# Kernel optimization log

Hardware: AMD Instinct MI355X
Metric: run time of the kernel (lower is better)

Reference implementation:

```python
import jax, jax.numpy as jnp
import numpy as np

N = 100000          # nodes (edges-as-nodes in ChiENN)
CIRCLE = 8          # circle_size
D_IN = 128
D_OUT = 128
K = 2               # k_neighbors -> padding = K - 1 = 1
PAD = K - 1


def setup_inputs() -> dict:
    key = jax.random.key(0)
    ks = jax.random.split(key, 8)
    x = jax.random.normal(ks[0], (N, D_IN), dtype=jnp.float32)
    # circle_index: per-row first `length` entries are valid node ids, tail is -1 padding
    lengths = jax.random.randint(ks[1], (N,), 0, CIRCLE + 1)  # 0..CIRCLE
    idx = jax.random.randint(ks[2], (N, CIRCLE), 0, N)
    pos = jnp.arange(CIRCLE)[None, :]
    circle_index = jnp.where(pos < lengths[:, None], idx, -1).astype(jnp.int64)
    s = 1.0 / np.sqrt(D_IN)
    w1 = jax.random.uniform(ks[3], (D_IN, D_OUT), jnp.float32, -s, s)
    b1 = jnp.zeros((D_OUT,), jnp.float32)
    w2 = jax.random.uniform(ks[4], (D_IN, D_OUT), jnp.float32, -s, s)
    b2 = jnp.zeros((D_OUT,), jnp.float32)
    sf = 1.0 / np.sqrt(D_OUT)
    wf = jax.random.uniform(ks[5], (D_OUT, D_OUT), jnp.float32, -sf, sf)
    bf = jnp.zeros((D_OUT,), jnp.float32)
    return {"x": x, "w1": w1, "b1": b1, "w2": w2, "b2": b2,
            "wf": wf, "bf": bf, "circle_index": circle_index}


def reference(x, w1, b1, w2, b2, wf, bf, circle_index):
    n, circle_size = circle_index.shape
    agg_id = 0.0  # aggregation_id_element for 'add'

    # per-shift embeddings of node features, each with a zero row prepended (index 0 = padding)
    embs = [x @ w1 + b1, x @ w2 + b2]                       # each [N, D]
    d = embs[0].shape[-1]
    zero_row = jnp.zeros((1, d), embs[0].dtype)
    embs = [jnp.concatenate([zero_row, e], axis=0) for e in embs]  # [N+1, D]

    mask_sum = jnp.sum(circle_index == -1, axis=-1)          # [N]
    in_degree = circle_size - mask_sum - PAD
    in_degree = jnp.where(mask_sum == circle_size, 0, in_degree)

    ci = circle_index.reshape(-1) + 1                        # [N*circle]  (-1 -> 0 = zero row)
    L = ci.shape[0]
    ci = jnp.concatenate([ci, jnp.zeros((PAD,), ci.dtype)])

    shifted = []
    for i, e in enumerate(embs):
        se = e[ci[i:i + L]]                                  # [L, D] circular-shifted gather
        # mask rows whose node in-degree <= shift i
        m = jnp.repeat(in_degree <= i, circle_size)[:, None]  # [L, 1]
        shifted.append(jnp.where(m, agg_id, se))
    msg = jnp.sum(jnp.stack(shifted, axis=-2), axis=-2)      # 'add' aggregation, [L, D]
    msg = msg.reshape(n, circle_size, d)

    msg_mask = jnp.arange(1, circle_size + 1)[None, :] <= in_degree[:, None]
    msg = msg[:, :-PAD, :]                                   # drop circular padding slots
    msg_mask = msg_mask[:, :-PAD]
    msg = jnp.where(msg_mask[..., None], msg, 0.0)
    msg = msg @ wf + bf                                      # final_embedding (Linear)
    return msg, msg_mask
```

## Files before the change

### kernel.cpp

```cpp
#include <hip/hip_runtime.h>
#include <stdint.h>

typedef short bf16x8 __attribute__((ext_vector_type(8)));
typedef float f32x4  __attribute__((ext_vector_type(4)));

__device__ __forceinline__ unsigned short f2bf(float f) {
    unsigned int u = __float_as_uint(f);
    u += 0x7FFFu + ((u >> 16) & 1u);
    return (unsigned short)(u >> 16);
}
__device__ __forceinline__ float bf2f(unsigned short h) {
    return __uint_as_float(((unsigned int)h) << 16);
}

__global__ void fuse_weights(const float* __restrict__ w1, const float* __restrict__ b1,
                             const float* __restrict__ w2, const float* __restrict__ b2,
                             const float* __restrict__ wf,
                             unsigned short* __restrict__ wcT,
                             float* __restrict__ cb)
{
    int mat = blockIdx.x / 129;
    int kk  = blockIdx.x % 129;
    int c   = threadIdx.x;
    const float* w = (mat == 0) ? w1 : w2;
    const float* b = (mat == 0) ? b1 : b2;
    float acc = 0.f;
    if (kk < 128) {
        #pragma unroll 8
        for (int j = 0; j < 128; ++j) acc += w[kk * 128 + j] * wf[j * 128 + c];
        wcT[mat * 16384 + c * 128 + kk] = f2bf(acc);
    } else {
        #pragma unroll 8
        for (int j = 0; j < 128; ++j) acc += b[j] * wf[j * 128 + c];
        cb[mat * 128 + c] = acc;
    }
}

#define WAVE_ROWS 32
__global__ __launch_bounds__(512) void gemm_g(
    const float* __restrict__ x, const unsigned short* __restrict__ wcT,
    const float* __restrict__ cb, unsigned short* __restrict__ g, int nrows)
{
    __shared__ uint4 ldsw[4096];

    int tid  = threadIdx.x;
    int lane = tid & 63;
    int wid  = tid >> 6;
    int r0   = (blockIdx.x * 8 + wid) * WAVE_ROWS;
    int lrow = lane & 15;
    int kg   = lane >> 4;
    int swz  = (lrow & 7) << 4;

    const uint4* w4 = (const uint4*)wcT;
    #pragma unroll
    for (int i = 0; i < 8; ++i) {
        int idx = tid + i * 512;
        uint4 v = w4[idx];
        int b   = idx << 4;
        int sb  = b ^ (((b >> 8) & 7) << 4);
        ldsw[sb >> 4] = v;
    }

    bf16x8 xf[2][4];
    #pragma unroll
    for (int t = 0; t < 2; ++t) {
        int row = r0 + t * 16 + lrow;
        bool v  = row < nrows;
        #pragma unroll
        for (int ks = 0; ks < 4; ++ks) {
            int k0 = ks * 32 + kg * 8;
            float4 p0 = v ? *(const float4*)(x + (size_t)row * 128 + k0)     : float4{0,0,0,0};
            float4 p1 = v ? *(const float4*)(x + (size_t)row * 128 + k0 + 4) : float4{0,0,0,0};
            bf16x8 f;
            f[0] = (short)f2bf(p0.x); f[1] = (short)f2bf(p0.y);
            f[2] = (short)f2bf(p0.z); f[3] = (short)f2bf(p0.w);
            f[4] = (short)f2bf(p1.x); f[5] = (short)f2bf(p1.y);
            f[6] = (short)f2bf(p1.z); f[7] = (short)f2bf(p1.w);
            xf[t][ks] = f;
        }
    }

    __syncthreads();
    if (r0 >= nrows) return;

    const char* lbase = (const char*)ldsw;
    #pragma unroll
    for (int mat = 0; mat < 2; ++mat) {
        unsigned short* gm = g + (size_t)mat * nrows * 128;
        int mb = mat * 32768;
        #pragma unroll 2
        for (int c = 0; c < 8; ++c) {
            int colb = mb + (c * 16 + lrow) * 256 + kg * 16;
            bf16x8 wfr[4];
            #pragma unroll
            for (int ks = 0; ks < 4; ++ks)
                wfr[ks] = *(const bf16x8*)(lbase + ((colb + ks * 64) ^ swz));
            f32x4 acc[2];
            #pragma unroll
            for (int t = 0; t < 2; ++t) acc[t] = f32x4{0,0,0,0};
            #pragma unroll
            for (int ks = 0; ks < 4; ++ks) {
                #pragma unroll
                for (int t = 0; t < 2; ++t)
                    acc[t] = __builtin_amdgcn_mfma_f32_16x16x32_bf16(wfr[ks], xf[t][ks], acc[t], 0,0,0);
            }
            float4 bias = *(const float4*)(cb + mat * 128 + c * 16 + kg * 4);
            #pragma unroll
            for (int t = 0; t < 2; ++t) {
                int xrow = r0 + t * 16 + lrow;
                if (xrow < nrows) {
                    ushort4 o;
                    o.x = f2bf(acc[t][0] + bias.x); o.y = f2bf(acc[t][1] + bias.y);
                    o.z = f2bf(acc[t][2] + bias.z); o.w = f2bf(acc[t][3] + bias.w);
                    *(ushort4*)(gm + (size_t)xrow * 128 + c * 16 + kg * 4) = o;
                }
            }
        }
    }
}

__global__ __launch_bounds__(256) void gather_out(
    const int* __restrict__ ci, const unsigned short* __restrict__ g,
    const float* __restrict__ bfv, float* __restrict__ out,
    float* __restrict__ maskout, int nnodes)
{
    int n    = (int)((blockIdx.x * blockDim.x + threadIdx.x) >> 6);
    int lane = threadIdx.x & 63;
    if (n >= nnodes) return;

    int civ = ci[n * 8 + (lane & 7)];
    unsigned long long bal = __ballot(civ == -1);
    int cnt = __popcll(bal & 0xFFull);
    int deg = (cnt == 8) ? 0 : (7 - cnt);

    int half = lane >> 5;
    int hl   = lane & 31;
    int d4   = hl * 4;
    float4 bfd = *(const float4*)(bfv + d4);
    const unsigned short* g1 = g;
    const unsigned short* g2 = g + (size_t)nnodes * 128;
    bool two = (deg >= 2);

    uint2 va[4], vb[4];
    #pragma unroll
    for (int c = 0; c < 4; ++c) {
        va[c] = uint2{0u, 0u};
        vb[c] = uint2{0u, 0u};
        if (2 * c < deg) {
            int r  = 2 * c + half;
            int i0 = __shfl(civ, r);
            int i1 = __shfl(civ, r + 1);
            bool m = (r < deg);
            va[c] = m          ? *(const uint2*)(g1 + (size_t)i0 * 128 + d4) : uint2{0u, 0u};
            vb[c] = (m && two) ? *(const uint2*)(g2 + (size_t)i1 * 128 + d4) : uint2{0u, 0u};
        }
    }

    size_t base = (size_t)n * 896;
    #pragma unroll
    for (int c = 0; c < 4; ++c) {
        f32x4 o;
        o[0] = bfd.x + bf2f((unsigned short)(va[c].x & 0xFFFFu)) + bf2f((unsigned short)(vb[c].x & 0xFFFFu));
        o[1] = bfd.y + bf2f((unsigned short)(va[c].x >> 16))     + bf2f((unsigned short)(vb[c].x >> 16));
        o[2] = bfd.z + bf2f((unsigned short)(va[c].y & 0xFFFFu)) + bf2f((unsigned short)(vb[c].y & 0xFFFFu));
        o[3] = bfd.w + bf2f((unsigned short)(va[c].y >> 16))     + bf2f((unsigned short)(vb[c].y >> 16));
        if (c < 3)
            __builtin_nontemporal_store(o, (f32x4*)(out + base + c * 256 + lane * 4));
        else if (half == 0)
            __builtin_nontemporal_store(o, (f32x4*)(out + base + 768 + hl * 4));
    }
    if (lane < 7)
        __builtin_nontemporal_store((lane < deg) ? 1.0f : 0.0f, maskout + n * 7 + lane);
}

extern "C" void kernel_launch(void* const* d_in, const int* in_sizes, int n_in,
                              void* d_out, int out_size, void* d_ws, size_t ws_size,
                              hipStream_t stream) {
    const float* x   = (const float*)d_in[0];
    const float* w1  = (const float*)d_in[1];
    const float* b1  = (const float*)d_in[2];
    const float* w2  = (const float*)d_in[3];
    const float* b2  = (const float*)d_in[4];
    const float* wf  = (const float*)d_in[5];
    const float* bfv = (const float*)d_in[6];
    const int*   ci  = (const int*)d_in[7];

    int nrows = in_sizes[0] / 128;

    size_t gbytes = (size_t)2 * nrows * 128 * 2;
    unsigned short* g   = (unsigned short*)d_ws;
    unsigned short* wcT = (unsigned short*)((char*)d_ws + ((gbytes + 255) & ~(size_t)255));
    float*          cb  = (float*)((char*)wcT + 2 * 128 * 128 * 2);

    fuse_weights<<<2 * 129, 128, 0, stream>>>(w1, b1, w2, b2, wf, wcT, cb);

    int nblk = (nrows + 8 * WAVE_ROWS - 1) / (8 * WAVE_ROWS);
    gemm_g<<<nblk, 512, 0, stream>>>(x, wcT, cb, g, nrows);

    int rows = nrows * 7;
    int cblk = (nrows * 64 + 255) / 256;
    float* out = (float*)d_out;
    gather_out<<<cblk, 256, 0, stream>>>(ci, g, bfv, out, out + (size_t)rows * 128, nrows);
}
```

Measured before the change: 112.1 us.

## Fuse three kernels into one persistent kernel with grid-wide barriers

Merges the weight-fusion, GEMM and gather kernels into a single persistent kernel launched with at most 448 blocks. The phases are separated by software grid barriers built on an atomic counter, which is reset by a memset before launch. The aim is to remove two kernel-launch gaps and the drain/fill between stages. In exchange it adds atomic spin-wait barriers, depends on every block being co-resident, and runs grid-stride loops with fewer blocks, which may lower gather parallelism.

```diff
diff --git a/kernel.cpp b/kernel.cpp
--- a/kernel.cpp
+++ b/kernel.cpp
@@ -13,164 +13,192 @@
     return __uint_as_float(((unsigned int)h) << 16);
 }
 
-__global__ void fuse_weights(const float* __restrict__ w1, const float* __restrict__ b1,
-                             const float* __restrict__ w2, const float* __restrict__ b2,
-                             const float* __restrict__ wf,
-                             unsigned short* __restrict__ wcT,
-                             float* __restrict__ cb)
-{
-    int mat = blockIdx.x / 129;
-    int kk  = blockIdx.x % 129;
-    int c   = threadIdx.x;
-    const float* w = (mat == 0) ? w1 : w2;
-    const float* b = (mat == 0) ? b1 : b2;
-    float acc = 0.f;
-    if (kk < 128) {
-        #pragma unroll 8
-        for (int j = 0; j < 128; ++j) acc += w[kk * 128 + j] * wf[j * 128 + c];
-        wcT[mat * 16384 + c * 128 + kk] = f2bf(acc);
-    } else {
-        #pragma unroll 8
-        for (int j = 0; j < 128; ++j) acc += b[j] * wf[j * 128 + c];
-        cb[mat * 128 + c] = acc;
-    }
-}
-
 #define WAVE_ROWS 32
-__global__ __launch_bounds__(512) void gemm_g(
-    const float* __restrict__ x, const unsigned short* __restrict__ wcT,
-    const float* __restrict__ cb, unsigned short* __restrict__ g, int nrows)
+
+__global__ __launch_bounds__(512, 4) void fused_all(
+    const float* __restrict__ x,
+    const float* __restrict__ w1, const float* __restrict__ b1,
+    const float* __restrict__ w2, const float* __restrict__ b2,
+    const float* __restrict__ wf, const float* __restrict__ bfv,
+    const int* __restrict__ ci,
+    unsigned short* __restrict__ wcT, float* __restrict__ cb,
+    unsigned short* __restrict__ gbuf,
+    float* __restrict__ out, float* __restrict__ maskout,
+    int nrows, int ntiles, int nblk, unsigned* __restrict__ bar)
 {
     __shared__ uint4 ldsw[4096];
-
     int tid  = threadIdx.x;
+    int bid  = blockIdx.x;
     int lane = tid & 63;
     int wid  = tid >> 6;
-    int r0   = (blockIdx.x * 8 + wid) * WAVE_ROWS;
-    int lrow = lane & 15;
-    int kg   = lane >> 4;
-    int swz  = (lrow & 7) << 4;
-
-    const uint4* w4 = (const uint4*)wcT;
-    #pragma unroll
-    for (int i = 0; i < 8; ++i) {
-        int idx = tid + i * 512;
-        uint4 v = w4[idx];
-        int b   = idx << 4;
-        int sb  = b ^ (((b >> 8) & 7) << 4);
-        ldsw[sb >> 4] = v;
-    }
-
-    bf16x8 xf[2][4];
-    #pragma unroll
-    for (int t = 0; t < 2; ++t) {
-        int row = r0 + t * 16 + lrow;
-        bool v  = row < nrows;
+
+    {
+        int tg = bid * 512 + tid;
+        if (tg < 258 * 128) {
+            int c   = tg & 127;
+            int job = tg >> 7;
+            int mat = (job >= 129) ? 1 : 0;
+            int kk  = job - mat * 129;
+            const float* w = mat ? w2 : w1;
+            const float* b = mat ? b2 : b1;
+            float acc = 0.f;
+            if (kk < 128) {
+                #pragma unroll 8
+                for (int j = 0; j < 128; ++j) acc += w[kk * 128 + j] * wf[j * 128 + c];
+                wcT[mat * 16384 + c * 128 + kk] = f2bf(acc);
+            } else {
+                #pragma unroll 8
+                for (int j = 0; j < 128; ++j) acc += b[j] * wf[j * 128 + c];
+                cb[mat * 128 + c] = acc;
+            }
+        }
+    }
+
+    __syncthreads();
+    if (tid == 0) {
+        __threadfence();
+        atomicAdd(bar, 1u);
+        while (__hip_atomic_load(bar, __ATOMIC_RELAXED, __HIP_MEMORY_SCOPE_AGENT)
+               < (unsigned)nblk)
+            __builtin_amdgcn_s_sleep(1);
+        __threadfence();
+    }
+    __syncthreads();
+
+    {
+        int lrow = lane & 15;
+        int kg   = lane >> 4;
+        int swz  = (lrow & 7) << 4;
+
+        const uint4* w4 = (const uint4*)wcT;
         #pragma unroll
-        for (int ks = 0; ks < 4; ++ks) {
-            int k0 = ks * 32 + kg * 8;
-            float4 p0 = v ? *(const float4*)(x + (size_t)row * 128 + k0)     : float4{0,0,0,0};
-            float4 p1 = v ? *(const float4*)(x + (size_t)row * 128 + k0 + 4) : float4{0,0,0,0};
-            bf16x8 f;
-            f[0] = (short)f2bf(p0.x); f[1] = (short)f2bf(p0.y);
-            f[2] = (short)f2bf(p0.z); f[3] = (short)f2bf(p0.w);
-            f[4] = (short)f2bf(p1.x); f[5] = (short)f2bf(p1.y);
-            f[6] = (short)f2bf(p1.z); f[7] = (short)f2bf(p1.w);
-            xf[t][ks] = f;
-        }
-    }
-
-    __syncthreads();
-    if (r0 >= nrows) return;
-
-    const char* lbase = (const char*)ldsw;
-    #pragma unroll
-    for (int mat = 0; mat < 2; ++mat) {
-        unsigned short* gm = g + (size_t)mat * nrows * 128;
-        int mb = mat * 32768;
-        #pragma unroll 2
-        for (int c = 0; c < 8; ++c) {
-            int colb = mb + (c * 16 + lrow) * 256 + kg * 16;
-            bf16x8 wfr[4];
-            #pragma unroll
-            for (int ks = 0; ks < 4; ++ks)
-                wfr[ks] = *(const bf16x8*)(lbase + ((colb + ks * 64) ^ swz));
-            f32x4 acc[2];
-            #pragma unroll
-            for (int t = 0; t < 2; ++t) acc[t] = f32x4{0,0,0,0};
-            #pragma unroll
-            for (int ks = 0; ks < 4; ++ks) {
+        for (int i = 0; i < 8; ++i) {
+            int idx = tid + i * 512;
+            uint4 v = w4[idx];
+            int b   = idx << 4;
+            int sb  = b ^ (((b >> 8) & 7) << 4);
+            ldsw[sb >> 4] = v;
+        }
+        __syncthreads();
+        const char* lbase = (const char*)ldsw;
+
+        for (int tile = bid; tile < ntiles; tile += nblk) {
+            int r0 = tile * 256 + wid * WAVE_ROWS;
+            if (r0 >= nrows) continue;
+
+            bf16x8 xf[2][4];
+            #pragma unroll
+            for (int t = 0; t < 2; ++t) {
+                int row = r0 + t * 16 + lrow;
+                bool v  = row < nrows;
                 #pragma unroll
-                for (int t = 0; t < 2; ++t)
-                    acc[t] = __builtin_amdgcn_mfma_f32_16x16x32_bf16(wfr[ks], xf[t][ks], acc[t], 0,0,0);
-            }
-            float4 bias = *(const float4*)(cb + mat * 128 + c * 16 + kg * 4);
-            #pragma unroll
-            for (int t = 0; t < 2; ++t) {
-                int xrow = r0 + t * 16 + lrow;
-                if (xrow < nrows) {
-                    ushort4 o;
-                    o.x = f2bf(acc[t][0] + bias.x); o.y = f2bf(acc[t][1] + bias.y);
-                    o.z = f2bf(acc[t][2] + bias.z); o.w = f2bf(acc[t][3] + bias.w);
-                    *(ushort4*)(gm + (size_t)xrow * 128 + c * 16 + kg * 4) = o;
+                for (int ks = 0; ks < 4; ++ks) {
+                    int k0 = ks * 32 + kg * 8;
+                    float4 p0 = v ? *(const float4*)(x + (size_t)row * 128 + k0)     : float4{0,0,0,0};
+                    float4 p1 = v ? *(const float4*)(x + (size_t)row * 128 + k0 + 4) : float4{0,0,0,0};
+                    bf16x8 f;
+                    f[0] = (short)f2bf(p0.x); f[1] = (short)f2bf(p0.y);
+                    f[2] = (short)f2bf(p0.z); f[3] = (short)f2bf(p0.w);
+                    f[4] = (short)f2bf(p1.x); f[5] = (short)f2bf(p1.y);
+                    f[6] = (short)f2bf(p1.z); f[7] = (short)f2bf(p1.w);
+                    xf[t][ks] = f;
                 }
             }
-        }
-    }
-}
-
-__global__ __launch_bounds__(256) void gather_out(
-    const int* __restrict__ ci, const unsigned short* __restrict__ g,
-    const float* __restrict__ bfv, float* __restrict__ out,
-    float* __restrict__ maskout, int nnodes)
-{
-    int n    = (int)((blockIdx.x * blockDim.x + threadIdx.x) >> 6);
-    int lane = threadIdx.x & 63;
-    if (n >= nnodes) return;
-
-    int civ = ci[n * 8 + (lane & 7)];
-    unsigned long long bal = __ballot(civ == -1);
-    int cnt = __popcll(bal & 0xFFull);
-    int deg = (cnt == 8) ? 0 : (7 - cnt);
-
-    int half = lane >> 5;
-    int hl   = lane & 31;
-    int d4   = hl * 4;
-    float4 bfd = *(const float4*)(bfv + d4);
-    const unsigned short* g1 = g;
-    const unsigned short* g2 = g + (size_t)nnodes * 128;
-    bool two = (deg >= 2);
-
-    uint2 va[4], vb[4];
-    #pragma unroll
-    for (int c = 0; c < 4; ++c) {
-        va[c] = uint2{0u, 0u};
-        vb[c] = uint2{0u, 0u};
-        if (2 * c < deg) {
-            int r  = 2 * c + half;
-            int i0 = __shfl(civ, r);
-            int i1 = __shfl(civ, r + 1);
-            bool m = (r < deg);
-            va[c] = m          ? *(const uint2*)(g1 + (size_t)i0 * 128 + d4) : uint2{0u, 0u};
-            vb[c] = (m && two) ? *(const uint2*)(g2 + (size_t)i1 * 128 + d4) : uint2{0u, 0u};
-        }
-    }
-
-    size_t base = (size_t)n * 896;
-    #pragma unroll
-    for (int c = 0; c < 4; ++c) {
-        f32x4 o;
-        o[0] = bfd.x + bf2f((unsigned short)(va[c].x & 0xFFFFu)) + bf2f((unsigned short)(vb[c].x & 0xFFFFu));
-        o[1] = bfd.y + bf2f((unsigned short)(va[c].x >> 16))     + bf2f((unsigned short)(vb[c].x >> 16));
-        o[2] = bfd.z + bf2f((unsigned short)(va[c].y & 0xFFFFu)) + bf2f((unsigned short)(vb[c].y & 0xFFFFu));
-        o[3] = bfd.w + bf2f((unsigned short)(va[c].y >> 16))     + bf2f((unsigned short)(vb[c].y >> 16));
-        if (c < 3)
-            __builtin_nontemporal_store(o, (f32x4*)(out + base + c * 256 + lane * 4));
-        else if (half == 0)
-            __builtin_nontemporal_store(o, (f32x4*)(out + base + 768 + hl * 4));
-    }
-    if (lane < 7)
-        __builtin_nontemporal_store((lane < deg) ? 1.0f : 0.0f, maskout + n * 7 + lane);
+
+            #pragma unroll
+            for (int mat = 0; mat < 2; ++mat) {
+                unsigned short* gm = gbuf + (size_t)mat * nrows * 128;
+                int mb = mat * 32768;
+                #pragma unroll 2
+                for (int c = 0; c < 8; ++c) {
+                    int colb = mb + (c * 16 + lrow) * 256 + kg * 16;
+                    bf16x8 wfr[4];
+                    #pragma unroll
+                    for (int ks = 0; ks < 4; ++ks)
+                        wfr[ks] = *(const bf16x8*)(lbase + ((colb + ks * 64) ^ swz));
+                    f32x4 acc[2];
+                    #pragma unroll
+                    for (int t = 0; t < 2; ++t) acc[t] = f32x4{0,0,0,0};
+                    #pragma unroll
+                    for (int ks = 0; ks < 4; ++ks) {
+                        #pragma unroll
+                        for (int t = 0; t < 2; ++t)
+                            acc[t] = __builtin_amdgcn_mfma_f32_16x16x32_bf16(wfr[ks], xf[t][ks], acc[t], 0,0,0);
+                    }
+                    float4 bias = *(const float4*)(cb + mat * 128 + c * 16 + kg * 4);
+                    #pragma unroll
+                    for (int t = 0; t < 2; ++t) {
+                        int xrow = r0 + t * 16 + lrow;
+                        if (xrow < nrows) {
+                            ushort4 o;
+                            o.x = f2bf(acc[t][0] + bias.x); o.y = f2bf(acc[t][1] + bias.y);
+                            o.z = f2bf(acc[t][2] + bias.z); o.w = f2bf(acc[t][3] + bias.w);
+                            *(ushort4*)(gm + (size_t)xrow * 128 + c * 16 + kg * 4) = o;
+                        }
+                    }
+                }
+            }
+        }
+    }
+
+    __syncthreads();
+    if (tid == 0) {
+        __threadfence();
+        atomicAdd(bar, 1u);
+        while (__hip_atomic_load(bar, __ATOMIC_RELAXED, __HIP_MEMORY_SCOPE_AGENT)
+               < (unsigned)(2 * nblk))
+            __builtin_amdgcn_s_sleep(1);
+        __threadfence();
+    }
+    __syncthreads();
+
+    {
+        const unsigned short* g1 = gbuf;
+        const unsigned short* g2 = gbuf + (size_t)nrows * 128;
+        int half = lane >> 5;
+        int hl   = lane & 31;
+        int d4   = hl * 4;
+        float4 bfd = *(const float4*)(bfv + d4);
+
+        for (int n = bid * 8 + wid; n < nrows; n += nblk * 8) {
+            int civ = ci[n * 8 + (lane & 7)];
+            unsigned long long bal = __ballot(civ == -1);
+            int cnt = __popcll(bal & 0xFFull);
+            int deg = (cnt == 8) ? 0 : (7 - cnt);
+            bool two = (deg >= 2);
+
+            uint2 va[4], vb[4];
+            #pragma unroll
+            for (int c = 0; c < 4; ++c) {
+                va[c] = uint2{0u, 0u};
+                vb[c] = uint2{0u, 0u};
+                if (2 * c < deg) {
+                    int r  = 2 * c + half;
+                    int i0 = __shfl(civ, r);
+                    int i1 = __shfl(civ, r + 1);
+                    bool m = (r < deg);
+                    va[c] = m          ? *(const uint2*)(g1 + (size_t)i0 * 128 + d4) : uint2{0u, 0u};
+                    vb[c] = (m && two) ? *(const uint2*)(g2 + (size_t)i1 * 128 + d4) : uint2{0u, 0u};
+                }
+            }
+
+            size_t base = (size_t)n * 896;
+            #pragma unroll
+            for (int c = 0; c < 4; ++c) {
+                f32x4 o;
+                o[0] = bfd.x + bf2f((unsigned short)(va[c].x & 0xFFFFu)) + bf2f((unsigned short)(vb[c].x & 0xFFFFu));
+                o[1] = bfd.y + bf2f((unsigned short)(va[c].x >> 16))     + bf2f((unsigned short)(vb[c].x >> 16));
+                o[2] = bfd.z + bf2f((unsigned short)(va[c].y & 0xFFFFu)) + bf2f((unsigned short)(vb[c].y & 0xFFFFu));
+                o[3] = bfd.w + bf2f((unsigned short)(va[c].y >> 16))     + bf2f((unsigned short)(vb[c].y >> 16));
+                if (c < 3)
+                    __builtin_nontemporal_store(o, (f32x4*)(out + base + c * 256 + lane * 4));
+                else if (half == 0)
+                    __builtin_nontemporal_store(o, (f32x4*)(out + base + 768 + hl * 4));
+            }
+            if (lane < 7)
+                __builtin_nontemporal_store((lane < deg) ? 1.0f : 0.0f, maskout + n * 7 + lane);
+        }
+    }
 }
 
 extern "C" void kernel_launch(void* const* d_in, const int* in_sizes, int n_in,
@@ -185,20 +213,21 @@
     const float* bfv = (const float*)d_in[6];
     const int*   ci  = (const int*)d_in[7];
 
-    int nrows = in_sizes[0] / 128;
+    int nrows  = in_sizes[0] / 128;
+    int ntiles = (nrows + 255) / 256;
+    int nblk   = ntiles < 448 ? ntiles : 448;
 
     size_t gbytes = (size_t)2 * nrows * 128 * 2;
     unsigned short* g   = (unsigned short*)d_ws;
     unsigned short* wcT = (unsigned short*)((char*)d_ws + ((gbytes + 255) & ~(size_t)255));
     float*          cb  = (float*)((char*)wcT + 2 * 128 * 128 * 2);
-
-    fuse_weights<<<2 * 129, 128, 0, stream>>>(w1, b1, w2, b2, wf, wcT, cb);
-
-    int nblk = (nrows + 8 * WAVE_ROWS - 1) / (8 * WAVE_ROWS);
-    gemm_g<<<nblk, 512, 0, stream>>>(x, wcT, cb, g, nrows);
+    unsigned*       bar = (unsigned*)((char*)cb + 1024);
+
+    hipMemsetAsync(bar, 0, 256, stream);
 
     int rows = nrows * 7;
-    int cblk = (nrows * 64 + 255) / 256;
     float* out = (float*)d_out;
-    gather_out<<<cblk, 256, 0, stream>>>(ci, g, bfv, out, out + (size_t)rows * 128, nrows);
-}
+    fused_all<<<nblk, 512, 0, stream>>>(x, w1, b1, w2, b2, wf, bfv, ci,
+                                        wcT, cb, g, out, out + (size_t)rows * 128,
+                                        nrows, ntiles, nblk, bar);
+}
```

New measurement: 190.4 us. 1.7x slower.
